# Optimization experiments

Hardware: AMD Instinct MI355X
Metric: run time of the kernel (lower is better)

The kernel has to match this reference:

```python
import jax, jax.numpy as jnp
import numpy as np

B, T, F, H = 16, 512, 32, 128
EPS = 1e-5


def _layer_norm(y, g, b):
    mu = jnp.mean(y, axis=-1, keepdims=True)
    var = jnp.mean(jnp.square(y - mu), axis=-1, keepdims=True)
    return (y - mu) * jax.lax.rsqrt(var + EPS) * g + b


def setup_inputs() -> dict:
    key = jax.random.key(0)
    ks = jax.random.split(key, 16)
    s = 0.1  # small param scale
    return {
        "x": jax.random.normal(ks[0], (B, T, F), jnp.float32),
        # weight GRN (input_size == hidden == F, skip is Identity)
        "wg_fc1_w": jax.random.normal(ks[1], (F, F), jnp.float32) * s,
        "wg_fc1_b": jnp.zeros((F,), jnp.float32),
        "wg_fc2_w": jax.random.normal(ks[2], (2 * F, F), jnp.float32) * s,
        "wg_fc2_b": jnp.zeros((2 * F,), jnp.float32),
        "wg_ln_g": jnp.ones((F,), jnp.float32),
        "wg_ln_b": jnp.zeros((F,), jnp.float32),
        # per-feature GRNs (input_size=1 -> hidden H), batched over F
        "f_fc1_w": jax.random.normal(ks[3], (F, H), jnp.float32) * s,   # torch Linear(1,H).weight squeezed
        "f_fc1_b": jax.random.normal(ks[4], (F, H), jnp.float32) * s,
        "f_fc2_w": jax.random.normal(ks[5], (F, 2 * H, H), jnp.float32) * s,
        "f_fc2_b": jax.random.normal(ks[6], (F, 2 * H), jnp.float32) * s,
        "f_skip_w": jax.random.normal(ks[7], (F, H), jnp.float32) * s,  # Linear(1,H).weight squeezed
        "f_skip_b": jax.random.normal(ks[8], (F, H), jnp.float32) * s,
        "f_ln_g": jnp.ones((F, H), jnp.float32),
        "f_ln_b": jnp.zeros((F, H), jnp.float32),
    }


def reference(x, wg_fc1_w, wg_fc1_b, wg_fc2_w, wg_fc2_b, wg_ln_g, wg_ln_b,
              f_fc1_w, f_fc1_b, f_fc2_w, f_fc2_b, f_skip_w, f_skip_b,
              f_ln_g, f_ln_b):
    # --- weight GRN over the feature axis: [B,T,F] -> [B,T,F] ---
    h = jax.nn.elu(jnp.einsum('btf,gf->btg', x, wg_fc1_w) + wg_fc1_b)
    h2 = jnp.einsum('btg,kg->btk', h, wg_fc2_w) + wg_fc2_b  # [B,T,2F]
    a, g = jnp.split(h2, 2, axis=-1)
    glu = a * jax.nn.sigmoid(g)
    weights = jax.nn.softmax(_layer_norm(x + glu, wg_ln_g, wg_ln_b), axis=-1)  # [B,T,F]

    # --- all F per-feature GRNs batched (input width 1) ---
    xe = x[..., None]                                   # [B,T,F,1]
    h = jax.nn.elu(xe * f_fc1_w + f_fc1_b)              # [B,T,F,H]
    h2 = jnp.einsum('btfh,fgh->btfg', h, f_fc2_w) + f_fc2_b  # [B,T,F,2H]
    a, g = jnp.split(h2, 2, axis=-1)
    glu = a * jax.nn.sigmoid(g)                         # [B,T,F,H]
    res = xe * f_skip_w + f_skip_b                      # [B,T,F,H]
    y = _layer_norm(res + glu, f_ln_g, f_ln_b)          # per-feature LN params [F,H]

    # --- softmax-weighted combine ---
    return jnp.einsum('btf,btfh->bth', weights, y)      # [B,T,H]
```

## Files before the change

kernel.cpp:

```cpp
#include <hip/hip_runtime.h>
#include <cstdint>
#include <cstddef>

#define EPS 1e-5f

typedef float    f4    __attribute__((ext_vector_type(4)));
typedef _Float16 half8 __attribute__((ext_vector_type(8)));
typedef _Float16 half4 __attribute__((ext_vector_type(4)));

#define S_XS 33
#define LOG2E 1.44269504088896f

#define GLD_LDS16(gp, lp)                                        \
    __builtin_amdgcn_global_load_lds(                            \
        (const __attribute__((address_space(1))) void*)(gp),     \
        (__attribute__((address_space(3))) void*)(lp), 16, 0, 0)

__device__ __forceinline__ float fexp(float x)  { return __builtin_amdgcn_exp2f(x * LOG2E); }
__device__ __forceinline__ float frcp(float x)  { return __builtin_amdgcn_rcpf(x); }
__device__ __forceinline__ float frsq(float x)  { return __builtin_amdgcn_rsqf(x); }
__device__ __forceinline__ float fsig(float g)  { return frcp(1.f + __builtin_amdgcn_exp2f(g * -LOG2E)); }
__device__ __forceinline__ float felu(float t)  { return t > 0.f ? t : fexp(t) - 1.f; }

__global__ __launch_bounds__(256) void k_prep(
    const float* __restrict__ in_w2, _Float16* __restrict__ w2c,
    const float* __restrict__ x, const float* __restrict__ w1,
    const float* __restrict__ b1, const float* __restrict__ w2,
    const float* __restrict__ b2, const float* __restrict__ lng,
    const float* __restrict__ lnb,
    float* __restrict__ x_t, float* __restrict__ wts_t)
{
    __shared__ float w1s[32 * S_XS];
    __shared__ float w2s[64 * S_XS];
    __shared__ float xsW[32 * S_XS];
    __shared__ float ytile[32 * S_XS];

    const int bid = blockIdx.x;
    const int tid = threadIdx.x;

    if (bid < 512) {
        int t = bid * 256 + tid;
        int q  = t & 3;
        int g  = (t >> 2) & 255;
        int fk = t >> 10;
        int f = fk >> 2, kq = fk & 3;
        const float* ip = in_w2 + ((size_t)f * 256 + g) * 128 + kq * 32 + q * 8;
        f4 v0 = *(const f4*)ip, v1 = *(const f4*)(ip + 4);
        half8 h;
        #pragma unroll
        for (int i = 0; i < 4; ++i) { h[i] = (_Float16)v0[i]; h[4 + i] = (_Float16)v1[i]; }
        *(half8*)(w2c + (size_t)fk * 8192 + q * 2048 + g * 8) = h;
        return;
    }

    const int lane = tid & 63;
    const int f = lane & 31;
    const int wv = tid >> 6;
    const int row0 = (bid - 512) * 32;

    for (int i = tid; i < 1024; i += 256) {
        int r = i >> 5, c = i & 31;
        w1s[r * S_XS + c] = w1[i];
        xsW[r * S_XS + c] = x[(size_t)row0 * 32 + i];
    }
    for (int i = tid; i < 2048; i += 256) {
        int r = i >> 5, c = i & 31;
        w2s[r * S_XS + c] = w2[i];
    }
    const float b1f = b1[f], b2a = b2[f], b2g = b2[f + 32];
    const float lgf = lng[f], lbf = lnb[f];
    __syncthreads();

    for (int rr = 0; rr < 8; ++rr) {
        const int r = wv * 8 + rr;
        float acc = b1f;
        #pragma unroll
        for (int k = 0; k < 32; ++k)
            acc = fmaf(w1s[f * S_XS + k], xsW[r * S_XS + k], acc);
        float hval = felu(acc);

        float a = b2a, g = b2g;
        #pragma unroll
        for (int k = 0; k < 32; ++k) {
            float hk = __shfl(hval, k, 64);
            a = fmaf(w2s[f * S_XS + k], hk, a);
            g = fmaf(w2s[(f + 32) * S_XS + k], hk, g);
        }
        float xv = xsW[r * S_XS + f];
        float v = xv + a * fsig(g);

        float s = v;
        #pragma unroll
        for (int o = 1; o < 64; o <<= 1) s += __shfl_xor(s, o, 64);
        float mu = s * (1.f / 64.f);
        float d = v - mu;
        float sq = d * d;
        #pragma unroll
        for (int o = 1; o < 64; o <<= 1) sq += __shfl_xor(sq, o, 64);
        float y = d * frsq(sq * (1.f / 64.f) + EPS) * lgf + lbf;

        float m = y;
        #pragma unroll
        for (int o = 1; o < 64; o <<= 1) m = fmaxf(m, __shfl_xor(m, o, 64));
        float e = fexp(y - m);
        float se = e;
        #pragma unroll
        for (int o = 1; o < 64; o <<= 1) se += __shfl_xor(se, o, 64);
        if (lane < 32) ytile[r * S_XS + f] = e * 2.f * frcp(se);
    }
    __syncthreads();
    for (int i = tid; i < 1024; i += 256) {
        int ff = i >> 5, r = i & 31;
        x_t[(size_t)ff * 8192 + row0 + r]   = xsW[r * S_XS + ff];
        wts_t[(size_t)ff * 8192 + row0 + r] = ytile[r * S_XS + ff];
    }
}

__global__ __launch_bounds__(256, 3) void k_main(
    const _Float16* __restrict__ w2c,
    const float* __restrict__ x_t,
    const float* __restrict__ wts_t,
    const float* __restrict__ fc1w, const float* __restrict__ fc1b,
    const float* __restrict__ fc2b,
    const float* __restrict__ skw, const float* __restrict__ skb,
    const float* __restrict__ lng, const float* __restrict__ lnb,
    float* __restrict__ out)
{
    __shared__ __align__(16) _Float16 bchunk[2][8192];

    const int tid = threadIdx.x;
    const int fbase = (blockIdx.x >> 7) * 4;
    const int row0 = (blockIdx.x & 127) * 64;

    const int lane = tid & 63;
    const int wv = tid >> 6;
    const int l15 = lane & 15;
    const int q = lane >> 4;
    const int boff = q * 2048 + l15 * 8;

    auto stage = [&](int c) {
        const _Float16* gp = w2c + ((size_t)(fbase + (c >> 2)) * 4 + (c & 3)) * 8192;
        #pragma unroll
        for (int r = 0; r < 4; ++r)
            GLD_LDS16(gp + (r * 256 + tid) * 8,
                      &bchunk[c & 1][(r * 256 + tid) * 8]);
    };

    float out_acc[8][4];
    #pragma unroll
    for (int nt = 0; nt < 8; ++nt)
        #pragma unroll
        for (int rg = 0; rg < 4; ++rg) out_acc[nt][rg] = 0.f;

    stage(0);
    __syncthreads();

    int c = 0;
    for (int fi = 0; fi < 4; ++fi) {
        const int f = fbase + fi;
        const float* xcol = x_t + (size_t)f * 8192 + row0 + wv * 16;
        const float* wcol = wts_t + (size_t)f * 8192 + row0 + wv * 16;
        const float xvA = xcol[l15];

        f4 acc[16];
        {
            f4 z; z[0] = 0.f; z[1] = 0.f; z[2] = 0.f; z[3] = 0.f;
            #pragma unroll
            for (int nt = 0; nt < 16; ++nt) acc[nt] = z;
        }

        #pragma unroll
        for (int kq = 0; kq < 4; ++kq, ++c) {
            if (c + 1 < 16) stage(c + 1);

            half8 A;
            {
                const float* wp = fc1w + f * 128 + kq * 32 + 8 * q;
                const float* bp = fc1b + f * 128 + kq * 32 + 8 * q;
                f4 w0 = *(const f4*)wp, w1v = *(const f4*)(wp + 4);
                f4 b0 = *(const f4*)bp, b1v = *(const f4*)(bp + 4);
                #pragma unroll
                for (int j = 0; j < 4; ++j) {
                    A[j]     = (_Float16)felu(fmaf(xvA, w0[j], b0[j]));
                    A[4 + j] = (_Float16)felu(fmaf(xvA, w1v[j], b1v[j]));
                }
            }

            const _Float16* bb = &bchunk[c & 1][boff];
            #pragma unroll
            for (int nt = 0; nt < 16; ++nt) {
                half8 B = *(const half8*)(bb + nt * 128);
                acc[nt] = __builtin_amdgcn_mfma_f32_16x16x32_f16(A, B, acc[nt], 0, 0, 0);
            }
            __syncthreads();
        }

        f4 xr = *(const f4*)(xcol + 4 * q);
        f4 wr = *(const f4*)(wcol + 4 * q);
        float s[4] = {0.f, 0.f, 0.f, 0.f}, sq[4] = {0.f, 0.f, 0.f, 0.f};
        #pragma unroll
        for (int nt = 0; nt < 8; ++nt) {
            const int h = nt * 16 + l15;
            float ba = fc2b[f * 256 + h];
            float bg = fc2b[f * 256 + 128 + h];
            float sw = skw[f * 128 + h];
            float sb = skb[f * 128 + h];
            #pragma unroll
            for (int rg = 0; rg < 4; ++rg) {
                float a = acc[nt][rg] + ba;
                float g = acc[nt + 8][rg] + bg;
                float val = fmaf(xr[rg], sw, sb) + a * fsig(g);
                acc[nt][rg] = val;
                s[rg] += val;
                sq[rg] = fmaf(val, val, sq[rg]);
            }
        }
        #pragma unroll
        for (int o = 1; o < 16; o <<= 1) {
            #pragma unroll
            for (int rg = 0; rg < 4; ++rg) {
                s[rg] += __shfl_xor(s[rg], o, 64);
                sq[rg] += __shfl_xor(sq[rg], o, 64);
            }
        }
        float mu[4], c1[4];
        #pragma unroll
        for (int rg = 0; rg < 4; ++rg) {
            mu[rg] = s[rg] * (1.f / 128.f);
            float var = sq[rg] * (1.f / 128.f) - mu[rg] * mu[rg];
            c1[rg] = wr[rg] * frsq(fmaxf(var, 0.f) + EPS);
        }
        #pragma unroll
        for (int nt = 0; nt < 8; ++nt) {
            const int h = nt * 16 + l15;
            float lg = lng[f * 128 + h];
            float lb = lnb[f * 128 + h];
            #pragma unroll
            for (int rg = 0; rg < 4; ++rg) {
                float u = (acc[nt][rg] - mu[rg]) * c1[rg];
                out_acc[nt][rg] = fmaf(u, lg, fmaf(wr[rg], lb, out_acc[nt][rg]));
            }
        }
    }

    #pragma unroll
    for (int nt = 0; nt < 8; ++nt) {
        #pragma unroll
        for (int rg = 0; rg < 4; ++rg) {
            const int r = row0 + wv * 16 + 4 * q + rg;
            atomicAdd(&out[(size_t)r * 128 + nt * 16 + l15], out_acc[nt][rg]);
        }
    }
}

extern "C" void kernel_launch(void* const* d_in, const int* in_sizes, int n_in,
                              void* d_out, int out_size, void* d_ws, size_t ws_size,
                              hipStream_t stream) {
    const float* x     = (const float*)d_in[0];
    const float* wg1w  = (const float*)d_in[1];
    const float* wg1b  = (const float*)d_in[2];
    const float* wg2w  = (const float*)d_in[3];
    const float* wg2b  = (const float*)d_in[4];
    const float* wglng = (const float*)d_in[5];
    const float* wglnb = (const float*)d_in[6];
    const float* fc1w  = (const float*)d_in[7];
    const float* fc1b  = (const float*)d_in[8];
    const float* fc2w  = (const float*)d_in[9];
    const float* fc2b  = (const float*)d_in[10];
    const float* skw   = (const float*)d_in[11];
    const float* skb   = (const float*)d_in[12];
    const float* lng   = (const float*)d_in[13];
    const float* lnb   = (const float*)d_in[14];
    float* out = (float*)d_out;

    char* ws = (char*)d_ws;
    _Float16* w2c = (_Float16*)ws;
    float* x_t    = (float*)(ws + (2u << 20));
    float* wts_t  = (float*)(ws + (3u << 20));

    k_prep<<<dim3(768), dim3(256), 0, stream>>>(fc2w, w2c, x, wg1w, wg1b,
                                                wg2w, wg2b, wglng, wglnb,
                                                x_t, wts_t);
    hipMemsetAsync(out, 0, (size_t)out_size * sizeof(float), stream);
    k_main<<<dim3(1024), dim3(256), 0, stream>>>(w2c, x_t, wts_t, fc1w, fc1b,
                                                 fc2b, skw, skb, lng, lnb, out);
}
```

Baseline: 170.2 us.

## Make weights block-resident per feature and replace atomics with fp16 partials plus reduce kernel

```diff
diff --git a/kernel.cpp b/kernel.cpp
--- a/kernel.cpp
+++ b/kernel.cpp
@@ -116,7 +116,7 @@
     }
 }
 
-__global__ __launch_bounds__(256, 3) void k_main(
+__global__ __launch_bounds__(256, 2) void k_main(
     const _Float16* __restrict__ w2c,
     const float* __restrict__ x_t,
     const float* __restrict__ wts_t,
@@ -124,13 +124,19 @@
     const float* __restrict__ fc2b,
     const float* __restrict__ skw, const float* __restrict__ skb,
     const float* __restrict__ lng, const float* __restrict__ lnb,
-    float* __restrict__ out)
+    _Float16* __restrict__ part)
 {
-    __shared__ __align__(16) _Float16 bchunk[2][8192];
+    __shared__ __align__(16) _Float16 w2s[4 * 8192];
 
     const int tid = threadIdx.x;
-    const int fbase = (blockIdx.x >> 7) * 4;
-    const int row0 = (blockIdx.x & 127) * 64;
+    const int f = blockIdx.x & 31;
+    const int tile = blockIdx.x >> 5;
+    const int row0 = tile * 512;
+
+    const _Float16* wsrc = w2c + (size_t)f * 32768;
+    #pragma unroll
+    for (int i = 0; i < 16; ++i)
+        GLD_LDS16(wsrc + (i * 256 + tid) * 8, &w2s[(i * 256 + tid) * 8]);
 
     const int lane = tid & 63;
     const int wv = tid >> 6;
@@ -138,78 +144,65 @@
     const int q = lane >> 4;
     const int boff = q * 2048 + l15 * 8;
 
-    auto stage = [&](int c) {
-        const _Float16* gp = w2c + ((size_t)(fbase + (c >> 2)) * 4 + (c & 3)) * 8192;
-        #pragma unroll
-        for (int r = 0; r < 4; ++r)
-            GLD_LDS16(gp + (r * 256 + tid) * 8,
-                      &bchunk[c & 1][(r * 256 + tid) * 8]);
-    };
-
-    float out_acc[8][4];
-    #pragma unroll
-    for (int nt = 0; nt < 8; ++nt)
-        #pragma unroll
-        for (int rg = 0; rg < 4; ++rg) out_acc[nt][rg] = 0.f;
-
-    stage(0);
+    float ba[8], bg[8], swv[8], sbv[8], lgv[8], lbv[8];
+    #pragma unroll
+    for (int nt = 0; nt < 8; ++nt) {
+        const int h = nt * 16 + l15;
+        ba[nt]  = fc2b[f * 256 + h];
+        bg[nt]  = fc2b[f * 256 + 128 + h];
+        swv[nt] = skw[f * 128 + h];
+        sbv[nt] = skb[f * 128 + h];
+        lgv[nt] = lng[f * 128 + h];
+        lbv[nt] = lnb[f * 128 + h];
+    }
+    const float* xcol = x_t + (size_t)f * 8192 + row0 + wv * 128;
+    const float* wcol = wts_t + (size_t)f * 8192 + row0 + wv * 128;
+    _Float16* pcol = part + ((size_t)f << 20) + row0 + wv * 128;
+
     __syncthreads();
 
-    int c = 0;
-    for (int fi = 0; fi < 4; ++fi) {
-        const int f = fbase + fi;
-        const float* xcol = x_t + (size_t)f * 8192 + row0 + wv * 16;
-        const float* wcol = wts_t + (size_t)f * 8192 + row0 + wv * 16;
-        const float xvA = xcol[l15];
+    for (int it = 0; it < 8; ++it) {
+        const int rb = it * 16;
+        const float xvA = xcol[rb + l15];
+
+        half8 A[4];
+        #pragma unroll
+        for (int kq = 0; kq < 4; ++kq) {
+            const float* wp = fc1w + f * 128 + kq * 32 + 8 * q;
+            const float* bp = fc1b + f * 128 + kq * 32 + 8 * q;
+            f4 w0 = *(const f4*)wp, w1v = *(const f4*)(wp + 4);
+            f4 b0 = *(const f4*)bp, b1v = *(const f4*)(bp + 4);
+            #pragma unroll
+            for (int j = 0; j < 4; ++j) {
+                A[kq][j]     = (_Float16)felu(fmaf(xvA, w0[j], b0[j]));
+                A[kq][4 + j] = (_Float16)felu(fmaf(xvA, w1v[j], b1v[j]));
+            }
+        }
 
         f4 acc[16];
-        {
-            f4 z; z[0] = 0.f; z[1] = 0.f; z[2] = 0.f; z[3] = 0.f;
-            #pragma unroll
-            for (int nt = 0; nt < 16; ++nt) acc[nt] = z;
-        }
-
-        #pragma unroll
-        for (int kq = 0; kq < 4; ++kq, ++c) {
-            if (c + 1 < 16) stage(c + 1);
-
-            half8 A;
-            {
-                const float* wp = fc1w + f * 128 + kq * 32 + 8 * q;
-                const float* bp = fc1b + f * 128 + kq * 32 + 8 * q;
-                f4 w0 = *(const f4*)wp, w1v = *(const f4*)(wp + 4);
-                f4 b0 = *(const f4*)bp, b1v = *(const f4*)(bp + 4);
-                #pragma unroll
-                for (int j = 0; j < 4; ++j) {
-                    A[j]     = (_Float16)felu(fmaf(xvA, w0[j], b0[j]));
-                    A[4 + j] = (_Float16)felu(fmaf(xvA, w1v[j], b1v[j]));
-                }
-            }
-
-            const _Float16* bb = &bchunk[c & 1][boff];
+        #pragma unroll
+        for (int nt = 0; nt < 8; ++nt)
+            #pragma unroll
+            for (int rg = 0; rg < 4; ++rg) { acc[nt][rg] = ba[nt]; acc[nt + 8][rg] = bg[nt]; }
+        #pragma unroll
+        for (int kq = 0; kq < 4; ++kq) {
+            const _Float16* bb = &w2s[kq * 8192 + boff];
             #pragma unroll
             for (int nt = 0; nt < 16; ++nt) {
                 half8 B = *(const half8*)(bb + nt * 128);
-                acc[nt] = __builtin_amdgcn_mfma_f32_16x16x32_f16(A, B, acc[nt], 0, 0, 0);
+                acc[nt] = __builtin_amdgcn_mfma_f32_16x16x32_f16(A[kq], B, acc[nt], 0, 0, 0);
             }
-            __syncthreads();
-        }
-
-        f4 xr = *(const f4*)(xcol + 4 * q);
-        f4 wr = *(const f4*)(wcol + 4 * q);
+        }
+
+        f4 xr = *(const f4*)(xcol + rb + 4 * q);
+        f4 wr = *(const f4*)(wcol + rb + 4 * q);
         float s[4] = {0.f, 0.f, 0.f, 0.f}, sq[4] = {0.f, 0.f, 0.f, 0.f};
         #pragma unroll
         for (int nt = 0; nt < 8; ++nt) {
-            const int h = nt * 16 + l15;
-            float ba = fc2b[f * 256 + h];
-            float bg = fc2b[f * 256 + 128 + h];
-            float sw = skw[f * 128 + h];
-            float sb = skb[f * 128 + h];
             #pragma unroll
             for (int rg = 0; rg < 4; ++rg) {
-                float a = acc[nt][rg] + ba;
-                float g = acc[nt + 8][rg] + bg;
-                float val = fmaf(xr[rg], sw, sb) + a * fsig(g);
+                float val = fmaf(xr[rg], swv[nt], sbv[nt])
+                          + acc[nt][rg] * fsig(acc[nt + 8][rg]);
                 acc[nt][rg] = val;
                 s[rg] += val;
                 sq[rg] = fmaf(val, val, sq[rg]);
@@ -230,26 +223,46 @@
             float var = sq[rg] * (1.f / 128.f) - mu[rg] * mu[rg];
             c1[rg] = wr[rg] * frsq(fmaxf(var, 0.f) + EPS);
         }
+
         #pragma unroll
         for (int nt = 0; nt < 8; ++nt) {
-            const int h = nt * 16 + l15;
-            float lg = lng[f * 128 + h];
-            float lb = lnb[f * 128 + h];
-            #pragma unroll
-            for (int rg = 0; rg < 4; ++rg) {
-                float u = (acc[nt][rg] - mu[rg]) * c1[rg];
-                out_acc[nt][rg] = fmaf(u, lg, fmaf(wr[rg], lb, out_acc[nt][rg]));
-            }
-        }
-    }
-
-    #pragma unroll
-    for (int nt = 0; nt < 8; ++nt) {
-        #pragma unroll
-        for (int rg = 0; rg < 4; ++rg) {
-            const int r = row0 + wv * 16 + 4 * q + rg;
-            atomicAdd(&out[(size_t)r * 128 + nt * 16 + l15], out_acc[nt][rg]);
-        }
+            half4 pk;
+            #pragma unroll
+            for (int rg = 0; rg < 4; ++rg)
+                pk[rg] = (_Float16)fmaf((acc[nt][rg] - mu[rg]) * c1[rg], lgv[nt],
+                                        wr[rg] * lbv[nt]);
+            *(half4*)(pcol + ((size_t)(nt * 16 + l15) << 13) + rb + 4 * q) = pk;
+        }
+    }
+}
+
+__global__ __launch_bounds__(256) void k_reduce(const _Float16* __restrict__ part,
+                                                float* __restrict__ out) {
+    __shared__ float t[16 * 129];
+    const int tid = threadIdx.x;
+    const int row0 = blockIdx.x * 16;
+    const int h = tid >> 1;
+    const int rbase = (tid & 1) * 8;
+
+    float acc[8] = {0.f, 0.f, 0.f, 0.f, 0.f, 0.f, 0.f, 0.f};
+    #pragma unroll
+    for (int fq = 0; fq < 32; ++fq) {
+        half8 v = *(const half8*)(part + (((size_t)fq * 128 + h) << 13) + row0 + rbase);
+        #pragma unroll
+        for (int j = 0; j < 8; ++j) acc[j] += (float)v[j];
+    }
+    #pragma unroll
+    for (int i = 0; i < 8; ++i) t[(rbase + i) * 129 + h] = acc[i];
+    __syncthreads();
+    const int hw = (tid & 31) * 4;
+    const int r0 = tid >> 5;
+    #pragma unroll
+    for (int p2 = 0; p2 < 2; ++p2) {
+        const int row = p2 * 8 + r0;
+        f4 o;
+        #pragma unroll
+        for (int j = 0; j < 4; ++j) o[j] = t[row * 129 + hw + j];
+        *(f4*)(out + (size_t)(row0 + row) * 128 + hw) = o;
     }
 }
 
@@ -274,14 +287,15 @@
     float* out = (float*)d_out;
 
     char* ws = (char*)d_ws;
-    _Float16* w2c = (_Float16*)ws;
-    float* x_t    = (float*)(ws + (2u << 20));
-    float* wts_t  = (float*)(ws + (3u << 20));
+    _Float16* w2c  = (_Float16*)ws;
+    float* x_t     = (float*)(ws + (2u << 20));
+    float* wts_t   = (float*)(ws + (3u << 20));
+    _Float16* part = (_Float16*)(ws + (4u << 20));
 
     k_prep<<<dim3(768), dim3(256), 0, stream>>>(fc2w, w2c, x, wg1w, wg1b,
                                                 wg2w, wg2b, wglng, wglnb,
                                                 x_t, wts_t);
-    hipMemsetAsync(out, 0, (size_t)out_size * sizeof(float), stream);
-    k_main<<<dim3(1024), dim3(256), 0, stream>>>(w2c, x_t, wts_t, fc1w, fc1b,
-                                                 fc2b, skw, skb, lng, lnb, out);
+    k_main<<<dim3(512), dim3(256), 0, stream>>>(w2c, x_t, wts_t, fc1w, fc1b,
+                                                fc2b, skw, skb, lng, lnb, part);
+    k_reduce<<<dim3(512), dim3(256), 0, stream>>>(part, out);
 }
```

Result: slower. 441.5 us (+159.4%).
